# Optimization experiments

Hardware: AMD Instinct MI355X
Metric: run time of the kernel (lower is better)

The kernel has to match this reference:

```python
import jax, jax.numpy as jnp
import numpy as np

N_NODES = 10000
N_EDGES = 320000
N_GSO = 2
BATCH = 4
F0, F1, F2 = 64, 128, 128
K = 3


def _spmm(rows, cols, vals, x_nbf):
    """Sparse GSO multiply: (S x) for x in node-major layout [N, B, F]."""
    src = x_nbf[cols] * vals[:, None, None]            # [E, B, F]
    return jax.ops.segment_sum(src, rows, num_segments=x_nbf.shape[0])


def _graph_filter(x, edge_index, edge_vals, W, b):
    """y = sum_e sum_k S_e^k x W[e,k] + b.
    x: [B, N, Fin]; edge_index: [E_gso, 2, nnz] int; edge_vals: [E_gso, nnz];
    W: [E_gso, K, Fin, Fout]; b: [Fout]."""
    z0 = x.transpose(1, 0, 2)                          # [N, B, Fin]
    n_gso, k_taps = W.shape[0], W.shape[1]
    out = jnp.zeros((z0.shape[0], z0.shape[1], W.shape[-1]), dtype=x.dtype)
    for e in range(n_gso):
        rows, cols = edge_index[e, 0], edge_index[e, 1]
        zk = z0                                        # tap k=0 is identity
        out = out + jnp.einsum('nbf,fg->nbg', zk, W[e, 0])
        for k in range(1, k_taps):
            zk = _spmm(rows, cols, edge_vals[e], zk)   # zk = S_e zk
            out = out + jnp.einsum('nbf,fg->nbg', zk, W[e, k])
    out = out + b
    return out.transpose(1, 0, 2)                      # [B, N, Fout]


def setup_inputs() -> dict:
    key = jax.random.key(0)
    ks = jax.random.split(key, 8)
    x = jax.random.normal(ks[0], (BATCH, N_NODES, F0), dtype=jnp.float32)
    edge_index = jax.random.randint(ks[1], (N_GSO, 2, N_EDGES), 0, N_NODES, dtype=jnp.int32)
    # scale edge values ~ 1/avg_degree to keep repeated diffusion stable
    edge_vals = jax.random.uniform(ks[2], (N_GSO, N_EDGES), dtype=jnp.float32) * (1.0 / 32.0)
    W1 = jax.random.normal(ks[3], (N_GSO, K, F0, F1), dtype=jnp.float32) * 0.05
    b1 = jax.random.normal(ks[4], (F1,), dtype=jnp.float32) * 0.05
    W2 = jax.random.normal(ks[5], (N_GSO, K, F1, F2), dtype=jnp.float32) * 0.05
    b2 = jax.random.normal(ks[6], (F2,), dtype=jnp.float32) * 0.05
    return {"x": x, "edge_index": edge_index, "edge_vals": edge_vals,
            "W1": W1, "b1": b1, "W2": W2, "b2": b2}


def reference(x, edge_index, edge_vals, W1, b1, W2, b2):
    h = _graph_filter(x, edge_index, edge_vals, W1, b1)
    h = _graph_filter(h, edge_index, edge_vals, W2, b2)
    return h[:, 0, :]                                  # idxTrainMovie = 0 -> [B, F2]
```

## Files before the change

kernel.cpp:

```cpp
#include <hip/hip_runtime.h>

#define N_NODES 10000
#define N_EDGES 320000
#define BCAP    96
#define NCPY    8
#define UNODES  80
#define UBLKS   125

__device__ __forceinline__ unsigned short f2bf(float x) {
    unsigned int u = __float_as_uint(x);
    unsigned int r = (u + 0x7fff + ((u >> 16) & 1)) >> 16;
    return (unsigned short)r;
}
__device__ __forceinline__ float bfhi(unsigned int u) { return __uint_as_float(u & 0xffff0000u); }

__global__ __launch_bounds__(256) void bucket_kernel(
        const int* __restrict__ ei, const float* __restrict__ ev,
        int* __restrict__ cnt, unsigned int* __restrict__ bkt,
        float* __restrict__ wA) {
    int part  = blockIdx.x & 7;
    int chunk = blockIdx.x >> 3;
    int base  = chunk * 2500;
    int e  = (base >= N_EDGES) ? 1 : 0;
    int t0 = base - e * N_EDGES;
    const int*   rp = ei + e * 2 * N_EDGES;
    const int*   cp = rp + N_EDGES;
    const float* vp = ev + e * N_EDGES;
    int clo = part * 1250;
    int koff = e ? 2 : 0;
    for (int i = threadIdx.x; i < 2500; i += 256) {
        int t = t0 + i;
        int c = cp[t];
        if ((unsigned)(c - clo) < 1250u) {
            int r = rp[t];
            float v = vp[t];
            int pos = atomicAdd(&cnt[e * N_NODES + c], 1);
            if (pos < BCAP)
                bkt[(e * N_NODES + c) * BCAP + pos] = ((unsigned int)f2bf(v) << 16) | (unsigned int)r;
            if (r == 0)
                atomicAdd(&wA[c * 4 + koff], v);
        }
    }
}

__global__ __launch_bounds__(256) void gstage1_kernel(
        const unsigned int* __restrict__ bkt, const int* __restrict__ cnt,
        float* __restrict__ wA) {
    int t = threadIdx.x;
    int gu = (blockIdx.x << 4) + (t >> 4);
    int li = t & 15;
    int e = (gu >= N_NODES) ? 1 : 0;
    int c = gu - e * N_NODES;
    int nc = cnt[e * N_NODES + c]; if (nc > BCAP) nc = BCAP;
    const unsigned int* bp = bkt + (e * N_NODES + c) * BCAP;
    int koff = e ? 2 : 0;
    float acc = 0.f;
    for (int p = li; p < nc; p += 16) {
        unsigned int u = bp[p];
        acc += bfhi(u) * wA[(u & 0xffff) * 4 + koff];
    }
    acc += __shfl_xor(acc, 1); acc += __shfl_xor(acc, 2);
    acc += __shfl_xor(acc, 4); acc += __shfl_xor(acc, 8);
    if (li == 0) wA[c * 4 + koff + 1] = acc;
}

__global__ __launch_bounds__(256) void gstage2_kernel(
        const unsigned int* __restrict__ bkt, const int* __restrict__ cnt,
        const float* __restrict__ wA, float4* __restrict__ wB0, float4* __restrict__ wB1) {
    int t = threadIdx.x;
    int gu = (blockIdx.x << 4) + (t >> 4);
    int li = t & 15;
    int e = (gu >= N_NODES) ? 1 : 0;
    int c = gu - e * N_NODES;
    int nc = cnt[e * N_NODES + c]; if (nc > BCAP) nc = BCAP;
    const unsigned int* bp = bkt + (e * N_NODES + c) * BCAP;
    const float4* wAp = (const float4*)wA;
    float x0 = 0.f, x1 = 0.f, x2 = 0.f;
    for (int p = li; p < nc; p += 16) {
        unsigned int u = bp[p];
        float v = bfhi(u);
        float4 wr = wAp[u & 0xffff];
        if (e == 0) { x0 += wr.y * v; x1 += wr.z * v; x2 += wr.w * v; }
        else        { x0 += wr.w * v; x1 += wr.x * v; x2 += wr.y * v; }
    }
    x0 += __shfl_xor(x0, 1); x0 += __shfl_xor(x0, 2); x0 += __shfl_xor(x0, 4); x0 += __shfl_xor(x0, 8);
    x1 += __shfl_xor(x1, 1); x1 += __shfl_xor(x1, 2); x1 += __shfl_xor(x1, 4); x1 += __shfl_xor(x1, 8);
    x2 += __shfl_xor(x2, 1); x2 += __shfl_xor(x2, 2); x2 += __shfl_xor(x2, 4); x2 += __shfl_xor(x2, 8);
    if (li == 0) {
        float4 o = make_float4(x0, x1, x2, 0.f);
        if (e == 0) wB0[c] = o; else wB1[c] = o;
    }
}

__global__ __launch_bounds__(256) void gstage3_kernel(
        const unsigned int* __restrict__ bkt, const int* __restrict__ cnt,
        const float4* __restrict__ wB0, const float4* __restrict__ wB1,
        float4* __restrict__ wC0, float4* __restrict__ wC1) {
    int t = threadIdx.x;
    int gu = (blockIdx.x << 4) + (t >> 4);
    int li = t & 15;
    int e = (gu >= N_NODES) ? 1 : 0;
    int c = gu - e * N_NODES;
    int nc = cnt[e * N_NODES + c]; if (nc > BCAP) nc = BCAP;
    const unsigned int* bp = bkt + (e * N_NODES + c) * BCAP;
    const float4* win = e ? wB1 : wB0;
    float x0 = 0.f, x1 = 0.f, x2 = 0.f;
    for (int p = li; p < nc; p += 16) {
        unsigned int u = bp[p];
        float v = bfhi(u);
        float4 wr = win[u & 0xffff];
        x0 += wr.x * v; x1 += wr.y * v; x2 += wr.z * v;
    }
    x0 += __shfl_xor(x0, 1); x0 += __shfl_xor(x0, 2); x0 += __shfl_xor(x0, 4); x0 += __shfl_xor(x0, 8);
    x1 += __shfl_xor(x1, 1); x1 += __shfl_xor(x1, 2); x1 += __shfl_xor(x1, 4); x1 += __shfl_xor(x1, 8);
    x2 += __shfl_xor(x2, 1); x2 += __shfl_xor(x2, 2); x2 += __shfl_xor(x2, 4); x2 += __shfl_xor(x2, 8);
    if (li == 0) {
        float4 o = make_float4(x0, x1, x2, 0.f);
        if (e == 0) wC0[c] = o; else wC1[c] = o;
    }
}

__global__ __launch_bounds__(256) void ugemm_kernel(const float* __restrict__ x,
                                                    const float* __restrict__ wA,
                                                    const float4* __restrict__ wB0,
                                                    const float4* __restrict__ wB1,
                                                    const float4* __restrict__ wC0,
                                                    const float4* __restrict__ wC1,
                                                    float* __restrict__ U8,
                                                    float* __restrict__ S8) {
    int t = threadIdx.x;
    int b = t >> 6, f = t & 63;
    int n0 = blockIdx.x * UNODES;
    int cp = blockIdx.x & (NCPY - 1);
    const float* xp = x + b * (N_NODES * 64) + f;
    const float4* wAp = (const float4*)wA;
    float acc[16];
    #pragma unroll
    for (int k = 0; k < 16; ++k) acc[k] = 0.f;
    float s0 = 0.f, s1 = 0.f, s2 = 0.f, s3 = 0.f;
    #pragma unroll 8
    for (int j = 0; j < UNODES; ++j) {
        int n = n0 + j;
        float4 a  = wAp[n];
        float4 p0 = wB0[n], p1 = wB1[n];
        float4 q0 = wC0[n], q1 = wC1[n];
        float xv = xp[n * 64];
        acc[0]  += a.x * xv;  acc[1]  += a.y * xv;
        acc[2]  += a.z * xv;  acc[3]  += a.w * xv;
        acc[4]  += p0.x * xv; acc[5]  += p0.y * xv; acc[6]  += p0.z * xv;
        acc[7]  += p1.x * xv; acc[8]  += p1.y * xv; acc[9]  += p1.z * xv;
        acc[10] += q0.x * xv; acc[11] += q0.y * xv; acc[12] += q0.z * xv;
        acc[13] += q1.x * xv; acc[14] += q1.y * xv; acc[15] += q1.z * xv;
        if (t == 0) { s0 += a.x; s1 += a.y; s2 += a.z; s3 += a.w; }
    }
    float* up = U8 + cp * 4096;
    #pragma unroll
    for (int k = 0; k < 16; ++k)
        atomicAdd(&up[k * 256 + t], acc[k]);
    if (t == 0) {
        float* sp = S8 + cp * 4;
        atomicAdd(&sp[0], s0); atomicAdd(&sp[1], s1);
        atomicAdd(&sp[2], s2); atomicAdd(&sp[3], s3);
    }
}

__global__ __launch_bounds__(512) void final_T_kernel(
        const float* __restrict__ x, const float* __restrict__ U8,
        const float* __restrict__ S8,
        const float* __restrict__ W1, const float* __restrict__ b1,
        float* __restrict__ T, float* __restrict__ out) {
    __shared__ float Ws[8192];
    __shared__ float src[256];
    int blk = blockIdx.x;
    int s = blk / 5, g = blk - s * 5;
    int t = threadIdx.x;
    if (blk == 0) out[t] = 0.f;
    const int w1off[5] = { 0, 8192, 16384, 32768, 40960 };
    const float4* wsrc = (const float4*)(W1 + w1off[s]);
    const float4* wsrc0 = (const float4*)(W1 + 24576);
    float4* wdst = (float4*)Ws;
    #pragma unroll
    for (int i = 0; i < 4; ++i) {
        float4 v = wsrc[i * 512 + t];
        if (s == 0) {
            float4 v2 = wsrc0[i * 512 + t];
            v.x += v2.x; v.y += v2.y; v.z += v2.z; v.w += v2.w;
        }
        wdst[i * 512 + t] = v;
    }
    if (t < 256) {
        const int hmap[5] = { -1, 0, 1, 2, 3 };
        const int umap[4][5] = {
            { 0, 1, 4,  8, 14 },
            { 1, 4, 10, 9, 15 },
            { 2, 5, 11, 3,  7 },
            { 3, 6, 12, 7, 13 },
        };
        int k = (g == 0) ? hmap[s] : umap[g - 1][s];
        float sv;
        if (k < 0) {
            sv = x[(t >> 6) * (N_NODES * 64) + (t & 63)];
        } else {
            sv = 0.f;
            #pragma unroll
            for (int c = 0; c < NCPY; ++c) sv += U8[c * 4096 + k * 256 + t];
        }
        src[t] = sv;
    }
    __syncthreads();
    int b = t >> 7, f1 = t & 127;
    const float* sp = src + b * 64;
    float acc = 0.f;
    #pragma unroll 16
    for (int f0 = 0; f0 < 64; ++f0)
        acc += sp[f0] * Ws[f0 * 128 + f1];
    if (s == 0) {
        if (g == 0) acc += b1[f1];
        else {
            float Sg = 0.f;
            #pragma unroll
            for (int c = 0; c < NCPY; ++c) Sg += S8[c * 4 + (g - 1)];
            acc += Sg * b1[f1];
        }
    }
    atomicAdd(&T[g * 512 + t], acc);
}

__global__ __launch_bounds__(512) void final_out_kernel(
        const float* __restrict__ T, const float* __restrict__ W2,
        const float* __restrict__ b2, float* __restrict__ out) {
    __shared__ float Ws[16384];
    __shared__ float Ts[512];
    int g = blockIdx.x;
    int t = threadIdx.x;
    const int w2off[5] = { 0, 16384, 32768, 65536, 81920 };
    const float4* wsrc = (const float4*)(W2 + w2off[g]);
    const float4* wsrc0 = (const float4*)(W2 + 49152);
    float4* wdst = (float4*)Ws;
    #pragma unroll
    for (int i = 0; i < 8; ++i) {
        float4 v = wsrc[i * 512 + t];
        if (g == 0) {
            float4 v2 = wsrc0[i * 512 + t];
            v.x += v2.x; v.y += v2.y; v.z += v2.z; v.w += v2.w;
        }
        wdst[i * 512 + t] = v;
    }
    Ts[t] = T[g * 512 + t];
    __syncthreads();
    int b = t >> 7, f2 = t & 127;
    const float* tp = Ts + b * 128;
    float acc = (g == 0) ? b2[f2] : 0.f;
    #pragma unroll 16
    for (int f1 = 0; f1 < 128; ++f1)
        acc += tp[f1] * Ws[f1 * 128 + f2];
    atomicAdd(&out[t], acc);
}

extern "C" void kernel_launch(void* const* d_in, const int* in_sizes, int n_in,
                              void* d_out, int out_size, void* d_ws, size_t ws_size,
                              hipStream_t stream) {
    const float* x  = (const float*)d_in[0];
    const int*   ei = (const int*)d_in[1];
    const float* ev = (const float*)d_in[2];
    const float* W1 = (const float*)d_in[3];
    const float* b1 = (const float*)d_in[4];
    const float* W2 = (const float*)d_in[5];
    const float* b2 = (const float*)d_in[6];
    float* out = (float*)d_out;

    char* ws = (char*)d_ws;
    size_t off = 0;
    auto alloc = [&](size_t bytes) { size_t o = off; off += (bytes + 255) & ~(size_t)255; return o; };
    size_t o_bkt   = alloc((size_t)2 * N_NODES * BCAP * 4);
    size_t o_zero  = off;
    size_t o_cnt   = alloc((size_t)2 * N_NODES * 4);
    size_t o_wA    = alloc((size_t)N_NODES * 4 * 4);
    size_t o_wB0   = alloc((size_t)N_NODES * 4 * 4);
    size_t o_wB1   = alloc((size_t)N_NODES * 4 * 4);
    size_t o_wC0   = alloc((size_t)N_NODES * 4 * 4);
    size_t o_wC1   = alloc((size_t)N_NODES * 4 * 4);
    size_t o_U     = alloc((size_t)NCPY * 16 * 256 * 4);
    size_t o_S     = alloc((size_t)NCPY * 4 * 4);
    size_t o_T     = alloc((size_t)5 * 512 * 4);
    size_t zero_bytes = off - o_zero;

    unsigned int* bkt = (unsigned int*)(ws + o_bkt);
    int*    cnt   = (int*)(ws + o_cnt);
    float*  wA    = (float*)(ws + o_wA);
    float4* wB0   = (float4*)(ws + o_wB0);
    float4* wB1   = (float4*)(ws + o_wB1);
    float4* wC0   = (float4*)(ws + o_wC0);
    float4* wC1   = (float4*)(ws + o_wC1);
    float*  U8    = (float*)(ws + o_U);
    float*  S8    = (float*)(ws + o_S);
    float*  T     = (float*)(ws + o_T);

    hipMemsetAsync(ws + o_zero, 0, zero_bytes, stream);

    bucket_kernel  <<<2048, 256, 0, stream>>>(ei, ev, cnt, bkt, wA);
    gstage1_kernel <<<1250, 256, 0, stream>>>(bkt, cnt, wA);
    gstage2_kernel <<<1250, 256, 0, stream>>>(bkt, cnt, wA, wB0, wB1);
    gstage3_kernel <<<1250, 256, 0, stream>>>(bkt, cnt, wB0, wB1, wC0, wC1);
    ugemm_kernel   <<<UBLKS, 256, 0, stream>>>(x, wA, wB0, wB1, wC0, wC1, U8, S8);
    final_T_kernel <<<25,   512, 0, stream>>>(x, U8, S8, W1, b1, T, out);
    final_out_kernel<<<5,   512, 0, stream>>>(T, W2, b2, out);
}
```

Baseline: 156.1 us.

## Build edge buckets in shared memory per column slice instead of global atomics

The bucketing kernel now gives each block a slice of 79 destination columns. Each block scans every column index of its GSO using int4 loads and fills its buckets with shared-memory atomics. It then writes the counts and bucket contents to global memory with plain coalesced stores, removing the global count atomics and scattered bucket writes. Because the counts are now written outright, the count and bucket buffers move out of the memset range, which shrinks the zeroing. The cost is that every block rereads the full column array, so redundant L2 traffic grows about 16x and only 256 blocks are launched.

```diff
diff --git a/kernel.cpp b/kernel.cpp
--- a/kernel.cpp
+++ b/kernel.cpp
@@ -6,6 +6,7 @@
 #define NCPY    8
 #define UNODES  80
 #define UBLKS   125
+#define PCOLS   79
 
 __device__ __forceinline__ unsigned short f2bf(float x) {
     unsigned int u = __float_as_uint(x);
@@ -18,29 +19,45 @@
         const int* __restrict__ ei, const float* __restrict__ ev,
         int* __restrict__ cnt, unsigned int* __restrict__ bkt,
         float* __restrict__ wA) {
-    int part  = blockIdx.x & 7;
-    int chunk = blockIdx.x >> 3;
-    int base  = chunk * 2500;
-    int e  = (base >= N_EDGES) ? 1 : 0;
-    int t0 = base - e * N_EDGES;
+    __shared__ unsigned int lbkt[PCOLS * BCAP];
+    __shared__ int lcnt[PCOLS];
+    int blk  = blockIdx.x;
+    int e    = blk >> 7;
+    int part = blk & 127;
+    int clo  = part * PCOLS;
+    int t = threadIdx.x;
+    for (int i = t; i < PCOLS; i += 256) lcnt[i] = 0;
+    __syncthreads();
     const int*   rp = ei + e * 2 * N_EDGES;
     const int*   cp = rp + N_EDGES;
     const float* vp = ev + e * N_EDGES;
-    int clo = part * 1250;
+    const int4*  cp4 = (const int4*)cp;
     int koff = e ? 2 : 0;
-    for (int i = threadIdx.x; i < 2500; i += 256) {
-        int t = t0 + i;
-        int c = cp[t];
-        if ((unsigned)(c - clo) < 1250u) {
-            int r = rp[t];
-            float v = vp[t];
-            int pos = atomicAdd(&cnt[e * N_NODES + c], 1);
-            if (pos < BCAP)
-                bkt[(e * N_NODES + c) * BCAP + pos] = ((unsigned int)f2bf(v) << 16) | (unsigned int)r;
-            if (r == 0)
-                atomicAdd(&wA[c * 4 + koff], v);
-        }
-    }
+    for (int i4 = t; i4 < N_EDGES / 4; i4 += 256) {
+        int4 c4 = cp4[i4];
+        #pragma unroll
+        for (int s = 0; s < 4; ++s) {
+            int c = (s == 0) ? c4.x : (s == 1) ? c4.y : (s == 2) ? c4.z : c4.w;
+            unsigned d = (unsigned)(c - clo);
+            if (d < PCOLS) {
+                int idx = i4 * 4 + s;
+                int r = rp[idx];
+                float v = vp[idx];
+                int pos = atomicAdd(&lcnt[d], 1);
+                if (pos < BCAP)
+                    lbkt[d * BCAP + pos] = ((unsigned int)f2bf(v) << 16) | (unsigned int)r;
+                if (r == 0)
+                    atomicAdd(&wA[c * 4 + koff], v);
+            }
+        }
+    }
+    __syncthreads();
+    int ncols = N_NODES - clo;
+    if (ncols > PCOLS) ncols = PCOLS;
+    for (int i = t; i < ncols; i += 256) cnt[e * N_NODES + clo + i] = lcnt[i];
+    int lim = ncols * BCAP;
+    unsigned int* gb = bkt + (size_t)(e * N_NODES + clo) * BCAP;
+    for (int i = t; i < lim; i += 256) gb[i] = lbkt[i];
 }
 
 __global__ __launch_bounds__(256) void gstage1_kernel(
@@ -272,18 +289,18 @@
     char* ws = (char*)d_ws;
     size_t off = 0;
     auto alloc = [&](size_t bytes) { size_t o = off; off += (bytes + 255) & ~(size_t)255; return o; };
+    size_t o_zero  = off;
+    size_t o_wA    = alloc((size_t)N_NODES * 4 * 4);
+    size_t o_U     = alloc((size_t)NCPY * 16 * 256 * 4);
+    size_t o_S     = alloc((size_t)NCPY * 4 * 4);
+    size_t o_T     = alloc((size_t)5 * 512 * 4);
+    size_t zero_bytes = off - o_zero;
     size_t o_bkt   = alloc((size_t)2 * N_NODES * BCAP * 4);
-    size_t o_zero  = off;
     size_t o_cnt   = alloc((size_t)2 * N_NODES * 4);
-    size_t o_wA    = alloc((size_t)N_NODES * 4 * 4);
     size_t o_wB0   = alloc((size_t)N_NODES * 4 * 4);
     size_t o_wB1   = alloc((size_t)N_NODES * 4 * 4);
     size_t o_wC0   = alloc((size_t)N_NODES * 4 * 4);
     size_t o_wC1   = alloc((size_t)N_NODES * 4 * 4);
-    size_t o_U     = alloc((size_t)NCPY * 16 * 256 * 4);
-    size_t o_S     = alloc((size_t)NCPY * 4 * 4);
-    size_t o_T     = alloc((size_t)5 * 512 * 4);
-    size_t zero_bytes = off - o_zero;
 
     unsigned int* bkt = (unsigned int*)(ws + o_bkt);
     int*    cnt   = (int*)(ws + o_cnt);
@@ -298,7 +315,7 @@
 
     hipMemsetAsync(ws + o_zero, 0, zero_bytes, stream);
 
-    bucket_kernel  <<<2048, 256, 0, stream>>>(ei, ev, cnt, bkt, wA);
+    bucket_kernel  <<<256,  256, 0, stream>>>(ei, ev, cnt, bkt, wA);
     gstage1_kernel <<<1250, 256, 0, stream>>>(bkt, cnt, wA);
     gstage2_kernel <<<1250, 256, 0, stream>>>(bkt, cnt, wA, wB0, wB1);
     gstage3_kernel <<<1250, 256, 0, stream>>>(bkt, cnt, wB0, wB1, wC0, wC1);
```

New measurement: 325.8 us. 109% more time.

## Precompose W1·W2 weight products inside bucket kernel and fuse final stages

Applied to the files above, without the earlier changes.

Adds 26 extra blocks to the bucket kernel that precompute the 25 combined W1×W2 matrices and the bias-propagation vectors, so this weight-only work overlaps the edge bucketing. The two final kernels (T then out, with atomics into a T buffer) become a single one-block kernel that applies the precomposed matrices to the 25 source vectors. This removes one launch and the atomic round trip, and shrinks the zeroed workspace. In exchange the final step runs in one block serially over 25 matrices read from global memory, and the extra blocks in the bucket kernel do uncoalesced W1 reads that could lengthen its tail.

```diff
diff --git a/kernel.cpp b/kernel.cpp
--- a/kernel.cpp
+++ b/kernel.cpp
@@ -17,7 +17,52 @@
 __global__ __launch_bounds__(256) void bucket_kernel(
         const int* __restrict__ ei, const float* __restrict__ ev,
         int* __restrict__ cnt, unsigned int* __restrict__ bkt,
-        float* __restrict__ wA) {
+        float* __restrict__ wA,
+        const float* __restrict__ W1, const float* __restrict__ b1,
+        const float* __restrict__ W2, const float* __restrict__ b2,
+        float* __restrict__ M, float* __restrict__ Nv) {
+    if (blockIdx.x >= 2048) {
+        int mb = blockIdx.x - 2048;
+        int t = threadIdx.x;
+        const int w2off[5] = { 0, 16384, 32768, 65536, 81920 };
+        if (mb < 25) {
+            int s = mb / 5, g = mb - s * 5;
+            const int w1off[5] = { 0, 8192, 16384, 32768, 40960 };
+            const float* w1p = W1 + w1off[s];
+            const float* w2p = W2 + w2off[g];
+            int f2 = t & 127;
+            int f0b = (t >> 7) * 32;
+            float acc[32];
+            #pragma unroll
+            for (int i = 0; i < 32; ++i) acc[i] = 0.f;
+            for (int f1 = 0; f1 < 128; ++f1) {
+                float w2v = w2p[f1 * 128 + f2];
+                if (g == 0) w2v += W2[49152 + f1 * 128 + f2];
+                #pragma unroll
+                for (int i = 0; i < 32; ++i) {
+                    float w1v = w1p[(f0b + i) * 128 + f1];
+                    if (s == 0) w1v += W1[24576 + (f0b + i) * 128 + f1];
+                    acc[i] += w1v * w2v;
+                }
+            }
+            float* mp = M + mb * 8192;
+            #pragma unroll
+            for (int i = 0; i < 32; ++i)
+                mp[(f0b + i) * 128 + f2] = acc[i];
+        } else if (t < 128) {
+            int f2 = t;
+            for (int g = 0; g < 5; ++g) {
+                float acc = (g == 0) ? b2[f2] : 0.f;
+                for (int f1 = 0; f1 < 128; ++f1) {
+                    float w2v = W2[w2off[g] + f1 * 128 + f2];
+                    if (g == 0) w2v += W2[49152 + f1 * 128 + f2];
+                    acc += b1[f1] * w2v;
+                }
+                Nv[g * 128 + f2] = acc;
+            }
+        }
+        return;
+    }
     int part  = blockIdx.x & 7;
     int chunk = blockIdx.x >> 3;
     int base  = chunk * 2500;
@@ -164,97 +209,53 @@
     }
 }
 
-__global__ __launch_bounds__(512) void final_T_kernel(
+__global__ __launch_bounds__(512) void final_kernel(
         const float* __restrict__ x, const float* __restrict__ U8,
         const float* __restrict__ S8,
-        const float* __restrict__ W1, const float* __restrict__ b1,
-        float* __restrict__ T, float* __restrict__ out) {
-    __shared__ float Ws[8192];
+        const float* __restrict__ M, const float* __restrict__ Nv,
+        float* __restrict__ out) {
     __shared__ float src[256];
-    int blk = blockIdx.x;
-    int s = blk / 5, g = blk - s * 5;
-    int t = threadIdx.x;
-    if (blk == 0) out[t] = 0.f;
-    const int w1off[5] = { 0, 8192, 16384, 32768, 40960 };
-    const float4* wsrc = (const float4*)(W1 + w1off[s]);
-    const float4* wsrc0 = (const float4*)(W1 + 24576);
-    float4* wdst = (float4*)Ws;
+    int t = threadIdx.x;
+    int b = t >> 7, f2 = t & 127;
+    const int kmap[25] = {
+        -1,  0,  1,  2,  3,
+         0,  1,  4,  5,  6,
+         1,  4, 10, 11, 12,
+         2,  8,  9,  3,  7,
+         3, 14, 15,  7, 13,
+    };
+    float Sg[4];
     #pragma unroll
-    for (int i = 0; i < 4; ++i) {
-        float4 v = wsrc[i * 512 + t];
-        if (s == 0) {
-            float4 v2 = wsrc0[i * 512 + t];
-            v.x += v2.x; v.y += v2.y; v.z += v2.z; v.w += v2.w;
+    for (int j = 0; j < 4; ++j) {
+        float a = 0.f;
+        #pragma unroll
+        for (int c = 0; c < NCPY; ++c) a += S8[c * 4 + j];
+        Sg[j] = a;
+    }
+    float acc = Nv[f2] + Sg[0] * Nv[128 + f2] + Sg[1] * Nv[256 + f2]
+                       + Sg[2] * Nv[384 + f2] + Sg[3] * Nv[512 + f2];
+    for (int mb = 0; mb < 25; ++mb) {
+        int k = kmap[mb];
+        if (t < 256) {
+            float sv;
+            if (k < 0) {
+                sv = x[(t >> 6) * (N_NODES * 64) + (t & 63)];
+            } else {
+                sv = 0.f;
+                #pragma unroll
+                for (int c = 0; c < NCPY; ++c) sv += U8[c * 4096 + k * 256 + t];
+            }
+            src[t] = sv;
         }
-        wdst[i * 512 + t] = v;
-    }
-    if (t < 256) {
-        const int hmap[5] = { -1, 0, 1, 2, 3 };
-        const int umap[4][5] = {
-            { 0, 1, 4,  8, 14 },
-            { 1, 4, 10, 9, 15 },
-            { 2, 5, 11, 3,  7 },
-            { 3, 6, 12, 7, 13 },
-        };
-        int k = (g == 0) ? hmap[s] : umap[g - 1][s];
-        float sv;
-        if (k < 0) {
-            sv = x[(t >> 6) * (N_NODES * 64) + (t & 63)];
-        } else {
-            sv = 0.f;
-            #pragma unroll
-            for (int c = 0; c < NCPY; ++c) sv += U8[c * 4096 + k * 256 + t];
-        }
-        src[t] = sv;
-    }
-    __syncthreads();
-    int b = t >> 7, f1 = t & 127;
-    const float* sp = src + b * 64;
-    float acc = 0.f;
-    #pragma unroll 16
-    for (int f0 = 0; f0 < 64; ++f0)
-        acc += sp[f0] * Ws[f0 * 128 + f1];
-    if (s == 0) {
-        if (g == 0) acc += b1[f1];
-        else {
-            float Sg = 0.f;
-            #pragma unroll
-            for (int c = 0; c < NCPY; ++c) Sg += S8[c * 4 + (g - 1)];
-            acc += Sg * b1[f1];
-        }
-    }
-    atomicAdd(&T[g * 512 + t], acc);
-}
-
-__global__ __launch_bounds__(512) void final_out_kernel(
-        const float* __restrict__ T, const float* __restrict__ W2,
-        const float* __restrict__ b2, float* __restrict__ out) {
-    __shared__ float Ws[16384];
-    __shared__ float Ts[512];
-    int g = blockIdx.x;
-    int t = threadIdx.x;
-    const int w2off[5] = { 0, 16384, 32768, 65536, 81920 };
-    const float4* wsrc = (const float4*)(W2 + w2off[g]);
-    const float4* wsrc0 = (const float4*)(W2 + 49152);
-    float4* wdst = (float4*)Ws;
-    #pragma unroll
-    for (int i = 0; i < 8; ++i) {
-        float4 v = wsrc[i * 512 + t];
-        if (g == 0) {
-            float4 v2 = wsrc0[i * 512 + t];
-            v.x += v2.x; v.y += v2.y; v.z += v2.z; v.w += v2.w;
-        }
-        wdst[i * 512 + t] = v;
-    }
-    Ts[t] = T[g * 512 + t];
-    __syncthreads();
-    int b = t >> 7, f2 = t & 127;
-    const float* tp = Ts + b * 128;
-    float acc = (g == 0) ? b2[f2] : 0.f;
-    #pragma unroll 16
-    for (int f1 = 0; f1 < 128; ++f1)
-        acc += tp[f1] * Ws[f1 * 128 + f2];
-    atomicAdd(&out[t], acc);
+        __syncthreads();
+        const float* mp = M + mb * 8192 + f2;
+        const float* sp = src + b * 64;
+        #pragma unroll 16
+        for (int f0 = 0; f0 < 64; ++f0)
+            acc += sp[f0] * mp[f0 * 128];
+        __syncthreads();
+    }
+    out[t] = acc;
 }
 
 extern "C" void kernel_launch(void* const* d_in, const int* in_sizes, int n_in,
@@ -276,14 +277,15 @@
     size_t o_zero  = off;
     size_t o_cnt   = alloc((size_t)2 * N_NODES * 4);
     size_t o_wA    = alloc((size_t)N_NODES * 4 * 4);
+    size_t o_U     = alloc((size_t)NCPY * 16 * 256 * 4);
+    size_t o_S     = alloc((size_t)NCPY * 4 * 4);
+    size_t zero_bytes = off - o_zero;
     size_t o_wB0   = alloc((size_t)N_NODES * 4 * 4);
     size_t o_wB1   = alloc((size_t)N_NODES * 4 * 4);
     size_t o_wC0   = alloc((size_t)N_NODES * 4 * 4);
     size_t o_wC1   = alloc((size_t)N_NODES * 4 * 4);
-    size_t o_U     = alloc((size_t)NCPY * 16 * 256 * 4);
-    size_t o_S     = alloc((size_t)NCPY * 4 * 4);
-    size_t o_T     = alloc((size_t)5 * 512 * 4);
-    size_t zero_bytes = off - o_zero;
+    size_t o_M     = alloc((size_t)25 * 8192 * 4);
+    size_t o_N     = alloc((size_t)5 * 128 * 4);
 
     unsigned int* bkt = (unsigned int*)(ws + o_bkt);
     int*    cnt   = (int*)(ws + o_cnt);
@@ -294,15 +296,15 @@
     float4* wC1   = (float4*)(ws + o_wC1);
     float*  U8    = (float*)(ws + o_U);
     float*  S8    = (float*)(ws + o_S);
-    float*  T     = (float*)(ws + o_T);
+    float*  M     = (float*)(ws + o_M);
+    float*  Nv    = (float*)(ws + o_N);
 
     hipMemsetAsync(ws + o_zero, 0, zero_bytes, stream);
 
-    bucket_kernel  <<<2048, 256, 0, stream>>>(ei, ev, cnt, bkt, wA);
+    bucket_kernel  <<<2074, 256, 0, stream>>>(ei, ev, cnt, bkt, wA, W1, b1, W2, b2, M, Nv);
     gstage1_kernel <<<1250, 256, 0, stream>>>(bkt, cnt, wA);
     gstage2_kernel <<<1250, 256, 0, stream>>>(bkt, cnt, wA, wB0, wB1);
     gstage3_kernel <<<1250, 256, 0, stream>>>(bkt, cnt, wB0, wB1, wC0, wC1);
     ugemm_kernel   <<<UBLKS, 256, 0, stream>>>(x, wA, wB0, wB1, wC0, wC1, U8, S8);
-    final_T_kernel <<<25,   512, 0, stream>>>(x, U8, S8, W1, b1, T, out);
-    final_out_kernel<<<5,   512, 0, stream>>>(T, W2, b2, out);
-}
+    final_kernel   <<<1,    512, 0, stream>>>(x, U8, S8, M, Nv, out);
+}
```

Result: slower. 565.6 us (+262.4%).
